# Performance work log

Hardware: AMD Instinct MI355X
Metric: run time of the kernel (lower is better)

The kernel has to match this reference:

```python
import jax, jax.numpy as jnp
import numpy as np

N_NODES = 100000
SELF_LOOP_W = 2.0  # improved=True in GCNConv -> A + 2I


def gcn_conv(x, src, dst, ew, W, b):
    """PyG GCNConv(improved=True): D^-1/2 (A + 2I) D^-1/2 X W + b.

    src/dst: edge endpoints, messages flow src -> dst (source_to_target).
    """
    n = x.shape[0]
    # degree after adding self loops with weight 2.0
    deg = jnp.zeros((n,), dtype=x.dtype).at[dst].add(ew) + SELF_LOOP_W
    dinv = jax.lax.rsqrt(deg)
    norm = dinv[src] * ew * dinv[dst]                      # [E]
    h = x @ W                                              # [N, out]
    agg = jax.ops.segment_sum(norm[:, None] * h[src], dst, num_segments=n)
    self_term = (SELF_LOOP_W * dinv * dinv)[:, None] * h   # self-loop edges
    return agg + self_term + b


def setup_inputs() -> dict:
    key = jax.random.key(0)
    ks = jax.random.split(key, 10)
    F_IN, H1, H2, C = 128, 128, 64, 5
    E = 1600000
    x = jax.random.normal(ks[0], (N_NODES, F_IN), dtype=jnp.float32)
    edge_index = jax.random.randint(ks[1], (2, E), 0, N_NODES, dtype=jnp.int64)
    edge_weight = jax.random.uniform(ks[2], (E,), dtype=jnp.float32)

    def glorot(k, shape):
        lim = float(np.sqrt(6.0 / (shape[0] + shape[1])))
        return jax.random.uniform(k, shape, jnp.float32, -lim, lim)

    return {
        "x": x,
        "edge_index": edge_index,
        "edge_weight": edge_weight,
        "W1": glorot(ks[3], (F_IN, H1)), "b1": jnp.zeros((H1,), jnp.float32),
        "W2": glorot(ks[4], (H1, H2)),  "b2": jnp.zeros((H2,), jnp.float32),
        "Wc": glorot(ks[5], (H2, C)),   "bc": jnp.zeros((C,), jnp.float32),
    }


def reference(x, edge_index, edge_weight, W1, b1, W2, b2, Wc, bc):
    src, dst = edge_index[0], edge_index[1]
    # conv1 + relu (dropout is identity in eval mode)
    h = jax.nn.relu(gcn_conv(x, src, dst, edge_weight, W1, b1))
    # conv2 + relu
    h = jax.nn.relu(gcn_conv(h, src, dst, edge_weight, W2, b2))
    # classifier head + log_softmax over classes
    logits = gcn_conv(h, src, dst, edge_weight, Wc, bc)
    return jax.nn.log_softmax(logits, axis=1)
```

## Files before the change

kernel.cpp:

```cpp
#include <hip/hip_runtime.h>
#include <hip/hip_bf16.h>

constexpr int TPB = 256;

static inline int cdiv(long long a, long long b) { return (int)((a + b - 1) / b); }

typedef __attribute__((ext_vector_type(8))) short bf16x8;
typedef __attribute__((ext_vector_type(4))) float f32x4;

__device__ inline unsigned short f2bf(float f) {
    __hip_bfloat16 h = __float2bfloat16(f);
    unsigned short u;
    __builtin_memcpy(&u, &h, 2);
    return u;
}

__device__ inline float bflo(unsigned u) { return __uint_as_float(u << 16); }
__device__ inline float bfhi(unsigned u) { return __uint_as_float(u & 0xffff0000u); }

__device__ inline unsigned relu_pk(unsigned w) {
    unsigned lo = (w & 0x8000u) ? 0u : (w & 0xFFFFu);
    unsigned hi = (w & 0x80000000u) ? 0u : (w & 0xFFFF0000u);
    return lo | hi;
}

constexpr int P1_CH   = 4096;
constexpr int MAXBINS = 512;
constexpr int BINCAP  = 4608;

__device__ __forceinline__ void part_body(const int* __restrict__ src,
                                          const int* __restrict__ dst,
                                          const float* __restrict__ ew,
                                          int* __restrict__ bincnt,
                                          int2* __restrict__ pbuf, int E, int nbins, int bid) {
    __shared__ int h[MAXBINS];
    for (int t = threadIdx.x; t < nbins; t += TPB) h[t] = 0;
    __syncthreads();
    const int lo = bid * P1_CH;
    const int hi = min(lo + P1_CH, E);
    for (int e = lo + threadIdx.x; e < hi; e += TPB)
        atomicAdd(&h[dst[e] >> 8], 1);
    __syncthreads();
    for (int t = threadIdx.x; t < nbins; t += TPB) {
        int c = h[t];
        h[t] = (c > 0) ? atomicAdd(&bincnt[t], c) : 0;
    }
    __syncthreads();
    for (int e = lo + threadIdx.x; e < hi; e += TPB) {
        int d = dst[e];
        int bin = d >> 8;
        int idx = atomicAdd(&h[bin], 1);
        if (idx < BINCAP)
            pbuf[(size_t)bin * BINCAP + idx] =
                make_int2((src[e] & 0x1FFFF) | ((d & 255) << 24), __float_as_int(ew[e]));
    }
}

template<int CAP>
__global__ __launch_bounds__(TPB) void k_bucket(const int2* __restrict__ pbuf,
                                                const int* __restrict__ bincnt,
                                                int2* __restrict__ pairs,
                                                int* __restrict__ cnt,
                                                float* __restrict__ dinv, int n) {
    __shared__ int   lcnt[TPB];
    __shared__ float ldeg[TPB];
    const int tid = threadIdx.x;
    lcnt[tid] = 0; ldeg[tid] = 0.f;
    __syncthreads();
    const int bin = blockIdx.x;
    const int m = min(bincnt[bin], BINCAP);
    const int2* pb = pbuf + (size_t)bin * BINCAP;
    for (int i = tid; i < m; i += TPB) {
        int2 pe = pb[i];
        int dlo = (pe.x >> 24) & 255;
        int s   = pe.x & 0x1FFFF;
        int pos = atomicAdd(&lcnt[dlo], 1);
        if (pos < CAP)
            pairs[(size_t)(bin * 256 + dlo) * CAP + pos] = make_int2(s, pe.y);
        atomicAdd(&ldeg[dlo], __int_as_float(pe.y));
    }
    __syncthreads();
    int node = bin * 256 + tid;
    if (node < n) {
        cnt[node]  = min(lcnt[tid], CAP);
        dinv[node] = rsqrtf(ldeg[tid] + 2.0f);
    }
}

template<int CAP>
__global__ void k_bucket_scatter(const int* __restrict__ src, const int* __restrict__ dst,
                                 const float* __restrict__ ew, int* __restrict__ cnt,
                                 int2* __restrict__ pairs, int E) {
    int e = blockIdx.x * TPB + threadIdx.x;
    if (e >= E) return;
    int d = dst[e];
    int pos = atomicAdd(&cnt[d], 1);
    if (pos < CAP)
        pairs[(size_t)d * CAP + pos] = make_int2(src[e], __float_as_int(ew[e]));
}

template<int CAP>
__global__ void k_deg(const int2* __restrict__ pairs, const int* __restrict__ cnt,
                      float* __restrict__ dinv, int n) {
    int node = blockIdx.x * (TPB / 64) + (threadIdx.x >> 6);
    if (node >= n) return;
    int lane = threadIdx.x & 63;
    int m = min(cnt[node], CAP);
    float v = 0.f;
    if (lane < m) v = __int_as_float(pairs[(size_t)node * CAP + lane].y);
#pragma unroll
    for (int d = 1; d < 64; d <<= 1) v += __shfl_xor(v, d);
    if (lane == 0) dinv[node] = rsqrtf(v + 2.0f);
}

template<int CAP>
__global__ void k_normw(int2* __restrict__ pairs, const int* __restrict__ cnt,
                        const float* __restrict__ dinv, int n) {
    int lane = threadIdx.x & 63;
    int g = lane >> 4, o = lane & 15;
    int wid = blockIdx.x * (TPB / 64) + (threadIdx.x >> 6);
    int node = wid * 4 + g;
    if (node >= n) return;
    int m = min(cnt[node], CAP);
    float dd = dinv[node];
    int2* pr = pairs + (size_t)node * CAP;
    for (int j = o; j < m; j += 16) {
        int2 p = pr[j];
        pr[j].y = __float_as_int(dinv[p.x] * __int_as_float(p.y) * dd);
    }
}


template<int KIN, int NCOL, bool RELU_IN, bool BF_IN>
__device__ __forceinline__ void gemm_mfma_body(const void* __restrict__ Xv,
                                               const float* __restrict__ W,
                                               __hip_bfloat16* __restrict__ H, int n, int bid) {
    constexpr int BM  = 128;
    constexpr int SX  = KIN + 8;
    constexpr int KCH = KIN / 32;
    constexpr int MT  = 4;
    constexpr int NT  = NCOL / 32;
    __shared__ short Xs[BM * SX];
    __shared__ short Ws[NCOL * SX];

    const int row0 = bid * BM;
    const int nrow = min(BM, n - row0);

    if constexpr (BF_IN) {
        const uint4* xg = (const uint4*)((const __hip_bfloat16*)Xv + (size_t)row0 * KIN);
        for (int i = threadIdx.x; i < BM * KIN / 8; i += TPB) {
            int r = i / (KIN / 8), c8 = i % (KIN / 8);
            uint4 v = make_uint4(0u, 0u, 0u, 0u);
            if (r < nrow) v = xg[i];
            if (RELU_IN) {
                v.x = relu_pk(v.x); v.y = relu_pk(v.y);
                v.z = relu_pk(v.z); v.w = relu_pk(v.w);
            }
            *(uint4*)&Xs[r * SX + c8 * 8] = v;
        }
    } else {
        const float4* xg = (const float4*)((const float*)Xv + (size_t)row0 * KIN);
        for (int i = threadIdx.x; i < BM * KIN / 4; i += TPB) {
            int r = i / (KIN / 4), c4 = i % (KIN / 4);
            float4 v = make_float4(0.f, 0.f, 0.f, 0.f);
            if (r < nrow) v = xg[i];
            if (RELU_IN) {
                v.x = fmaxf(v.x, 0.f); v.y = fmaxf(v.y, 0.f);
                v.z = fmaxf(v.z, 0.f); v.w = fmaxf(v.w, 0.f);
            }
            ushort4 b;
            b.x = f2bf(v.x); b.y = f2bf(v.y);
            b.z = f2bf(v.z); b.w = f2bf(v.w);
            *(ushort4*)&Xs[r * SX + c4 * 4] = b;
        }
    }
    for (int i = threadIdx.x; i < KIN * NCOL; i += TPB) {
        int k = i / NCOL, c = i % NCOL;
        Ws[c * SX + k] = (short)f2bf(W[i]);
    }
    __syncthreads();

    const int wave = threadIdx.x >> 6;
    const int lane = threadIdx.x & 63;
    const int wr = wave >> 1;
    const int wc = wave & 1;
    const int fr = lane & 15;
    const int fg = lane >> 4;

    f32x4 acc[MT][NT];
#pragma unroll
    for (int i = 0; i < MT; ++i)
#pragma unroll
        for (int j = 0; j < NT; ++j) acc[i][j] = (f32x4){0.f, 0.f, 0.f, 0.f};

    const short* xa = Xs + (wr * 64 + fr) * SX + fg * 8;
    const short* wb = Ws + (wc * NT * 16 + fr) * SX + fg * 8;

#pragma unroll
    for (int kc = 0; kc < KCH; ++kc) {
        bf16x8 a[MT], b[NT];
#pragma unroll
        for (int i = 0; i < MT; ++i)
            a[i] = *(const bf16x8*)(xa + i * 16 * SX + kc * 32);
#pragma unroll
        for (int j = 0; j < NT; ++j)
            b[j] = *(const bf16x8*)(wb + j * 16 * SX + kc * 32);
#pragma unroll
        for (int i = 0; i < MT; ++i)
#pragma unroll
            for (int j = 0; j < NT; ++j)
                acc[i][j] = __builtin_amdgcn_mfma_f32_16x16x32_bf16(a[i], b[j], acc[i][j], 0, 0, 0);
    }

#pragma unroll
    for (int i = 0; i < MT; ++i) {
#pragma unroll
        for (int j = 0; j < NT; ++j) {
            int col = wc * NT * 16 + j * 16 + fr;
            int rb  = wr * 64 + i * 16 + fg * 4;
#pragma unroll
            for (int q = 0; q < 4; ++q) {
                int r = rb + q;
                if (r < nrow)
                    H[(size_t)(row0 + r) * NCOL + col] = __float2bfloat16(acc[i][j][q]);
            }
        }
    }
}

template<int KIN, int NCOL, bool RELU_IN, bool BF_IN>
__global__ __launch_bounds__(TPB, 2) void k_gemm_mfma(const void* __restrict__ Xv,
                                                      const float* __restrict__ W,
                                                      __hip_bfloat16* __restrict__ H, int n) {
    gemm_mfma_body<KIN, NCOL, RELU_IN, BF_IN>(Xv, W, H, n, blockIdx.x);
}

__global__ __launch_bounds__(TPB, 2) void k_gemm1_part(
        const float* __restrict__ X, const float* __restrict__ W1,
        __hip_bfloat16* __restrict__ H, int n,
        const int* __restrict__ src, const int* __restrict__ dst,
        const float* __restrict__ ew, int* __restrict__ bincnt,
        int2* __restrict__ pbuf, int E, int nbins, int Gg, int Gp) {
    int b = blockIdx.x;
    int r3 = b % 3;
    if (r3 == 2) {
        int pid = b / 3;
        if (pid < Gp) part_body(src, dst, ew, bincnt, pbuf, E, nbins, pid);
    } else {
        int gid = (b / 3) * 2 + r3;
        if (gid < Gg) gemm_mfma_body<128, 128, false, false>(X, W1, H, n, gid);
    }
}

template<int KIN, int KOUT, int OSTR, bool RELU_IN>
__global__ void k_gemv(const float* __restrict__ X, const float* __restrict__ W,
                       float* __restrict__ H, int n) {
    __shared__ float ws_[KIN * KOUT];
    for (int i = threadIdx.x; i < KIN * KOUT; i += TPB) ws_[i] = W[i];
    __syncthreads();
    int r = blockIdx.x * TPB + threadIdx.x;
    if (r >= n) return;
    float acc[KOUT];
#pragma unroll
    for (int c = 0; c < KOUT; ++c) acc[c] = 0.f;
    const float4* xr = (const float4*)(X + (size_t)r * KIN);
#pragma unroll
    for (int k4 = 0; k4 < KIN / 4; ++k4) {
        float4 xv = xr[k4];
        if (RELU_IN) {
            xv.x = fmaxf(xv.x, 0.f); xv.y = fmaxf(xv.y, 0.f);
            xv.z = fmaxf(xv.z, 0.f); xv.w = fmaxf(xv.w, 0.f);
        }
        float xs[4] = {xv.x, xv.y, xv.z, xv.w};
#pragma unroll
        for (int j = 0; j < 4; ++j)
#pragma unroll
            for (int c = 0; c < KOUT; ++c)
                acc[c] = fmaf(xs[j], ws_[(k4 * 4 + j) * KOUT + c], acc[c]);
    }
#pragma unroll
    for (int c = 0; c < KOUT; ++c) H[(size_t)r * OSTR + c] = acc[c];
#pragma unroll
    for (int c = KOUT; c < OSTR; ++c) H[(size_t)r * OSTR + c] = 0.f;
}


template<int K, int CAP, bool OUT_BF16>
__global__ __launch_bounds__(TPB) void k_agg_bf(const __hip_bfloat16* __restrict__ H,
                                                const int2* __restrict__ pairs,
                                                const int* __restrict__ cnt,
                                                const float* __restrict__ dinv,
                                                const float* __restrict__ b,
                                                void* __restrict__ out, int n) {
    constexpr int LPN = K / 8;
    constexpr int GPN = 64 / LPN;
    constexpr int RQ  = K / 8;
    constexpr int NCH = CAP / 8;
    const int lane = threadIdx.x & 63;
    const int g    = lane / LPN;
    const int o    = lane % LPN;
    const int wid  = blockIdx.x * (TPB / 64) + (threadIdx.x >> 6);
    const int node = wid * GPN + g;
    const bool alive = node < n;
    const int nc = alive ? node : 0;

    const uint4* __restrict__ Hq = (const uint4*)H;

    float di   = dinv[nc];
    float coef = 2.f * di * di;
    uint4 hv = Hq[(size_t)nc * RQ + o];
    const float4* bq = (const float4*)b + o * 2;
    float4 bA = bq[0], bB = bq[1];
    float acc[8];
    acc[0] = fmaf(coef, bflo(hv.x), bA.x);
    acc[1] = fmaf(coef, bfhi(hv.x), bA.y);
    acc[2] = fmaf(coef, bflo(hv.y), bA.z);
    acc[3] = fmaf(coef, bfhi(hv.y), bA.w);
    acc[4] = fmaf(coef, bflo(hv.z), bB.x);
    acc[5] = fmaf(coef, bfhi(hv.z), bB.y);
    acc[6] = fmaf(coef, bflo(hv.w), bB.z);
    acc[7] = fmaf(coef, bfhi(hv.w), bB.w);

    const int m = alive ? min(cnt[nc], CAP) : 0;
    const int2* pp = pairs + (size_t)nc * CAP;

    uint4 Ma[4], Mb[4];
#pragma unroll
    for (int q = 0; q < 4; ++q) Ma[q] = *(const uint4*)(pp + q * 2);

    auto chunk = [&](const uint4 (&Mc)[4], uint4 (&Mn)[4], int c) {
        const int base = c * 8;
        int s[8]; float w[8];
#pragma unroll
        for (int q = 0; q < 4; ++q) {
            s[2 * q]     = (int)Mc[q].x;  w[2 * q]     = __uint_as_float(Mc[q].y);
            s[2 * q + 1] = (int)Mc[q].z;  w[2 * q + 1] = __uint_as_float(Mc[q].w);
        }
        uint4 r[8];
#pragma unroll
        for (int u = 0; u < 8; ++u) {
            bool ok = (base + u) < m;
            int ss = ok ? s[u] : 0;
            if (!ok) w[u] = 0.f;
            r[u] = Hq[(size_t)ss * RQ + o];
        }
        if (base + 8 < m) {
#pragma unroll
            for (int q = 0; q < 4; ++q) Mn[q] = *(const uint4*)(pp + base + 8 + q * 2);
        }
#pragma unroll
        for (int u = 0; u < 8; ++u) {
            acc[0] = fmaf(w[u], bflo(r[u].x), acc[0]);
            acc[1] = fmaf(w[u], bfhi(r[u].x), acc[1]);
            acc[2] = fmaf(w[u], bflo(r[u].y), acc[2]);
            acc[3] = fmaf(w[u], bfhi(r[u].y), acc[3]);
            acc[4] = fmaf(w[u], bflo(r[u].z), acc[4]);
            acc[5] = fmaf(w[u], bfhi(r[u].z), acc[5]);
            acc[6] = fmaf(w[u], bflo(r[u].w), acc[6]);
            acc[7] = fmaf(w[u], bfhi(r[u].w), acc[7]);
        }
    };

#pragma unroll
    for (int c = 0; c < NCH; c += 2) {
        if (c * 8 >= m) break;
        chunk(Ma, Mb, c);
        if ((c + 1) * 8 >= m) break;
        chunk(Mb, Ma, c + 1);
    }

    if (alive) {
        if constexpr (OUT_BF16) {
            unsigned p0 = (unsigned)f2bf(acc[0]) | ((unsigned)f2bf(acc[1]) << 16);
            unsigned p1 = (unsigned)f2bf(acc[2]) | ((unsigned)f2bf(acc[3]) << 16);
            unsigned p2 = (unsigned)f2bf(acc[4]) | ((unsigned)f2bf(acc[5]) << 16);
            unsigned p3 = (unsigned)f2bf(acc[6]) | ((unsigned)f2bf(acc[7]) << 16);
            ((uint4*)out)[(size_t)node * RQ + o] = make_uint4(p0, p1, p2, p3);
        } else {
            float4* ap = (float4*)out + (size_t)node * (K / 4) + o * 2;
            ap[0] = make_float4(acc[0], acc[1], acc[2], acc[3]);
            ap[1] = make_float4(acc[4], acc[5], acc[6], acc[7]);
        }
    }
}

template<int CAP>
__global__ void k_agg5_lsm(const float* __restrict__ H, const int2* __restrict__ pairs,
                           const int* __restrict__ cnt, const float* __restrict__ dinv,
                           const float* __restrict__ b, float* __restrict__ out, int n) {
    constexpr int NCH = CAP / 8;
    int i = blockIdx.x * TPB + threadIdx.x;
    const bool alive = i < n;
    const int nc = alive ? i : 0;
    float di = dinv[nc];
    float coef = 2.f * di * di;
    float acc[5];
    {
        const float4 h0 = *(const float4*)(H + (size_t)nc * 8);
        const float  h4 = H[(size_t)nc * 8 + 4];
        acc[0] = fmaf(coef, h0.x, b[0]);
        acc[1] = fmaf(coef, h0.y, b[1]);
        acc[2] = fmaf(coef, h0.z, b[2]);
        acc[3] = fmaf(coef, h0.w, b[3]);
        acc[4] = fmaf(coef, h4,   b[4]);
    }
    const int m = alive ? min(cnt[nc], CAP) : 0;
    const int2* pp = pairs + (size_t)nc * CAP;

    uint4 Ma[4], Mb[4];
#pragma unroll
    for (int q = 0; q < 4; ++q) Ma[q] = *(const uint4*)(pp + q * 2);

    auto chunk = [&](const uint4 (&Mc)[4], uint4 (&Mn)[4], int c) {
        const int base = c * 8;
        int s[8]; float w[8];
#pragma unroll
        for (int q = 0; q < 4; ++q) {
            s[2 * q]     = (int)Mc[q].x;  w[2 * q]     = __uint_as_float(Mc[q].y);
            s[2 * q + 1] = (int)Mc[q].z;  w[2 * q + 1] = __uint_as_float(Mc[q].w);
        }
        float4 q0[8]; float q4[8];
#pragma unroll
        for (int u = 0; u < 8; ++u) {
            bool ok = (base + u) < m;
            int ss = ok ? s[u] : 0;
            if (!ok) w[u] = 0.f;
            const float* h = H + (size_t)ss * 8;
            q0[u] = *(const float4*)h;
            q4[u] = h[4];
        }
        if (base + 8 < m) {
#pragma unroll
            for (int q = 0; q < 4; ++q) Mn[q] = *(const uint4*)(pp + base + 8 + q * 2);
        }
#pragma unroll
        for (int u = 0; u < 8; ++u) {
            acc[0] = fmaf(w[u], q0[u].x, acc[0]);
            acc[1] = fmaf(w[u], q0[u].y, acc[1]);
            acc[2] = fmaf(w[u], q0[u].z, acc[2]);
            acc[3] = fmaf(w[u], q0[u].w, acc[3]);
            acc[4] = fmaf(w[u], q4[u],   acc[4]);
        }
    };

#pragma unroll
    for (int c = 0; c < NCH; c += 2) {
        if (c * 8 >= m) break;
        chunk(Ma, Mb, c);
        if ((c + 1) * 8 >= m) break;
        chunk(Mb, Ma, c + 1);
    }

    if (alive) {
        float mx = acc[0];
#pragma unroll
        for (int c = 1; c < 5; ++c) mx = fmaxf(mx, acc[c]);
        float ssum = 0.f;
#pragma unroll
        for (int c = 0; c < 5; ++c) ssum += expf(acc[c] - mx);
        float lg = mx + logf(ssum);
#pragma unroll
        for (int c = 0; c < 5; ++c) out[(size_t)i * 5 + c] = acc[c] - lg;
    }
}


template<int CAP>
static void run_all(const float* x, const int* srcv, const int* dstv, const float* ew,
                    const float* W1, const float* b1, const float* W2, const float* b2,
                    const float* Wc, const float* bc, float* out,
                    int n, int E, char* p, hipStream_t stream) {
    auto alloc = [&](size_t bytes) {
        char* r = p;
        p += (bytes + 255) & ~(size_t)255;
        return r;
    };
    float*          dinv   = (float*)alloc((size_t)n * 4);
    int*            cnt    = (int*)alloc((size_t)n * 4);
    int2*           pairs  = (int2*)alloc((size_t)n * CAP * 8);
    __hip_bfloat16* Hbf    = (__hip_bfloat16*)alloc((size_t)n * 128 * 2);
    __hip_bfloat16* A1bf   = (__hip_bfloat16*)alloc((size_t)n * 128 * 2);
    float*          bufB   = (float*)alloc((size_t)n * 64 * 4);
    float*          H3     = (float*)alloc((size_t)n * 8 * 4);
    int*            bincnt = (int*)alloc((size_t)MAXBINS * 4);
    int2*           pbuf   = (int2*)alloc((size_t)MAXBINS * BINCAP * 8);

    const int WPB = TPB / 64;
    const int nbins = cdiv(n, 256);

    if (nbins <= MAXBINS) {
        (void)hipMemsetAsync(bincnt, 0, (size_t)nbins * 4, stream);
        int Gg = cdiv(n, 128);
        int Gp = cdiv(E, P1_CH);
        int Gh = cdiv(Gg, 2);
        int G  = 3 * (Gp > Gh ? Gp : Gh);
        k_gemm1_part<<<G, TPB, 0, stream>>>(x, W1, Hbf, n, srcv, dstv, ew,
                                            bincnt, pbuf, E, nbins, Gg, Gp);
        k_bucket<CAP><<<nbins, TPB, 0, stream>>>(pbuf, bincnt, pairs, cnt, dinv, n);
    } else {
        (void)hipMemsetAsync(cnt, 0, (size_t)n * 4, stream);
        k_bucket_scatter<CAP><<<cdiv(E, TPB), TPB, 0, stream>>>(srcv, dstv, ew, cnt, pairs, E);
        k_deg<CAP><<<cdiv(n, WPB), TPB, 0, stream>>>(pairs, cnt, dinv, n);
        k_gemm_mfma<128, 128, false, false><<<cdiv(n, 128), TPB, 0, stream>>>(x, W1, Hbf, n);
    }
    k_normw<CAP><<<cdiv(n, WPB * 4), TPB, 0, stream>>>(pairs, cnt, dinv, n);

    k_agg_bf<128, CAP, true><<<cdiv(n, WPB * 4), TPB, 0, stream>>>(Hbf, pairs, cnt, dinv, b1, A1bf, n);

    k_gemm_mfma<128, 64, true, true><<<cdiv(n, 128), TPB, 0, stream>>>(A1bf, W2, Hbf, n);
    k_agg_bf<64, CAP, false><<<cdiv(n, WPB * 8), TPB, 0, stream>>>(Hbf, pairs, cnt, dinv, b2, bufB, n);

    k_gemv<64, 5, 8, true><<<cdiv(n, TPB), TPB, 0, stream>>>(bufB, Wc, H3, n);
    k_agg5_lsm<CAP><<<cdiv(n, TPB), TPB, 0, stream>>>(H3, pairs, cnt, dinv, bc, out, n);
}

extern "C" void kernel_launch(void* const* d_in, const int* in_sizes, int n_in,
                              void* d_out, int out_size, void* d_ws, size_t ws_size,
                              hipStream_t stream) {
    const float* x  = (const float*)d_in[0];
    const int*   ei = (const int*)d_in[1];
    const float* ew = (const float*)d_in[2];
    const float* W1 = (const float*)d_in[3];
    const float* b1 = (const float*)d_in[4];
    const float* W2 = (const float*)d_in[5];
    const float* b2 = (const float*)d_in[6];
    const float* Wc = (const float*)d_in[7];
    const float* bc = (const float*)d_in[8];

    const int E   = in_sizes[2];
    const int H1  = in_sizes[4];
    const int FIN = in_sizes[3] / H1;
    const int n   = in_sizes[0] / FIN;

    const int* srcv = ei;
    const int* dstv = ei + E;

    size_t fixed = ((size_t)n * 4 + 256) * 2 + ((size_t)n * 128 * 2 + 256) * 2 +
                   (size_t)n * 64 * 4 + 256 + (size_t)n * 8 * 4 + 256 +
                   (size_t)MAXBINS * 4 + 256 + (size_t)MAXBINS * BINCAP * 8 + 256 + 1024;
    if (ws_size == 0 || ws_size >= fixed + (size_t)n * 64 * 8)
        run_all<64>(x, srcv, dstv, ew, W1, b1, W2, b2, Wc, bc, (float*)d_out, n, E,
                    (char*)d_ws, stream);
    else
        run_all<48>(x, srcv, dstv, ew, W1, b1, W2, b2, Wc, bc, (float*)d_out, n, E,
                    (char*)d_ws, stream);
}
```

Measured before the change: 217.0 us.

## Drop normalized-weight pass, compute edge norms in aggregation, stage bucket writes in LDS

Removes the k_normw pass that rewrote each edge weight as dinv[src]*w*dinv[dst]. The three aggregation kernels now gather dinv[src] per edge and apply the normalization inline. k_bucket now does a prefix scan and stages edges in shared memory so the writes to pairs are contiguous rather than atomic-scattered. The fused gemm1+partition kernel is split back into separate launches, which gives up the overlap it provided but frees the bucket kernel's larger shared-memory use. The trade is an extra random dinv gather per edge in each of three layers, against one fewer full pass over the edge list.

After: 231.3 us. 1.07x slower.

```diff
diff --git a/kernel.cpp b/kernel.cpp
--- a/kernel.cpp
+++ b/kernel.cpp
@@ -28,15 +28,15 @@
 constexpr int MAXBINS = 512;
 constexpr int BINCAP  = 4608;
 
-__device__ __forceinline__ void part_body(const int* __restrict__ src,
-                                          const int* __restrict__ dst,
-                                          const float* __restrict__ ew,
-                                          int* __restrict__ bincnt,
-                                          int2* __restrict__ pbuf, int E, int nbins, int bid) {
+__global__ __launch_bounds__(TPB) void k_part(const int* __restrict__ src,
+                                              const int* __restrict__ dst,
+                                              const float* __restrict__ ew,
+                                              int* __restrict__ bincnt,
+                                              int2* __restrict__ pbuf, int E, int nbins) {
     __shared__ int h[MAXBINS];
     for (int t = threadIdx.x; t < nbins; t += TPB) h[t] = 0;
     __syncthreads();
-    const int lo = bid * P1_CH;
+    const int lo = blockIdx.x * P1_CH;
     const int hi = min(lo + P1_CH, E);
     for (int e = lo + threadIdx.x; e < hi; e += TPB)
         atomicAdd(&h[dst[e] >> 8], 1);
@@ -62,10 +62,15 @@
                                                 int2* __restrict__ pairs,
                                                 int* __restrict__ cnt,
                                                 float* __restrict__ dinv, int n) {
-    __shared__ int   lcnt[TPB];
-    __shared__ float ldeg[TPB];
+    __shared__ int   lcnt[256];
+    __shared__ int   loff[256];
+    __shared__ int   posc[256];
+    __shared__ float ldeg[256];
+    __shared__ int   scan_[256];
+    __shared__ int2  sbuf[BINCAP];
+    __shared__ unsigned char dbin[BINCAP];
     const int tid = threadIdx.x;
-    lcnt[tid] = 0; ldeg[tid] = 0.f;
+    lcnt[tid] = 0; ldeg[tid] = 0.f; posc[tid] = 0;
     __syncthreads();
     const int bin = blockIdx.x;
     const int m = min(bincnt[bin], BINCAP);
@@ -73,16 +78,42 @@
     for (int i = tid; i < m; i += TPB) {
         int2 pe = pb[i];
         int dlo = (pe.x >> 24) & 255;
-        int s   = pe.x & 0x1FFFF;
-        int pos = atomicAdd(&lcnt[dlo], 1);
-        if (pos < CAP)
-            pairs[(size_t)(bin * 256 + dlo) * CAP + pos] = make_int2(s, pe.y);
+        atomicAdd(&lcnt[dlo], 1);
         atomicAdd(&ldeg[dlo], __int_as_float(pe.y));
     }
     __syncthreads();
+    const int c = min(lcnt[tid], CAP);
+    scan_[tid] = c;
+    __syncthreads();
+#pragma unroll
+    for (int off = 1; off < 256; off <<= 1) {
+        int t = 0;
+        if (tid >= off) t = scan_[tid - off];
+        __syncthreads();
+        if (tid >= off) scan_[tid] += t;
+        __syncthreads();
+    }
+    loff[tid] = scan_[tid] - c;
+    __syncthreads();
+    const int total = scan_[255];
+    for (int i = tid; i < m; i += TPB) {
+        int2 pe = pb[i];
+        int dlo = (pe.x >> 24) & 255;
+        int slot = atomicAdd(&posc[dlo], 1);
+        if (slot < CAP) {
+            int j = loff[dlo] + slot;
+            sbuf[j] = make_int2(pe.x & 0x1FFFF, pe.y);
+            dbin[j] = (unsigned char)dlo;
+        }
+    }
+    __syncthreads();
+    for (int j = tid; j < total; j += TPB) {
+        int dlo = dbin[j];
+        pairs[(size_t)(bin * 256 + dlo) * CAP + (j - loff[dlo])] = sbuf[j];
+    }
     int node = bin * 256 + tid;
     if (node < n) {
-        cnt[node]  = min(lcnt[tid], CAP);
+        cnt[node]  = c;
         dinv[node] = rsqrtf(ldeg[tid] + 2.0f);
     }
 }
@@ -113,28 +144,11 @@
     if (lane == 0) dinv[node] = rsqrtf(v + 2.0f);
 }
 
-template<int CAP>
-__global__ void k_normw(int2* __restrict__ pairs, const int* __restrict__ cnt,
-                        const float* __restrict__ dinv, int n) {
-    int lane = threadIdx.x & 63;
-    int g = lane >> 4, o = lane & 15;
-    int wid = blockIdx.x * (TPB / 64) + (threadIdx.x >> 6);
-    int node = wid * 4 + g;
-    if (node >= n) return;
-    int m = min(cnt[node], CAP);
-    float dd = dinv[node];
-    int2* pr = pairs + (size_t)node * CAP;
-    for (int j = o; j < m; j += 16) {
-        int2 p = pr[j];
-        pr[j].y = __float_as_int(dinv[p.x] * __int_as_float(p.y) * dd);
-    }
-}
-
 
 template<int KIN, int NCOL, bool RELU_IN, bool BF_IN>
-__device__ __forceinline__ void gemm_mfma_body(const void* __restrict__ Xv,
-                                               const float* __restrict__ W,
-                                               __hip_bfloat16* __restrict__ H, int n, int bid) {
+__global__ __launch_bounds__(TPB, 2) void k_gemm_mfma(const void* __restrict__ Xv,
+                                                      const float* __restrict__ W,
+                                                      __hip_bfloat16* __restrict__ H, int n) {
     constexpr int BM  = 128;
     constexpr int SX  = KIN + 8;
     constexpr int KCH = KIN / 32;
@@ -143,7 +157,7 @@
     __shared__ short Xs[BM * SX];
     __shared__ short Ws[NCOL * SX];
 
-    const int row0 = bid * BM;
+    const int row0 = blockIdx.x * BM;
     const int nrow = min(BM, n - row0);
 
     if constexpr (BF_IN) {
@@ -225,30 +239,6 @@
                     H[(size_t)(row0 + r) * NCOL + col] = __float2bfloat16(acc[i][j][q]);
             }
         }
-    }
-}
-
-template<int KIN, int NCOL, bool RELU_IN, bool BF_IN>
-__global__ __launch_bounds__(TPB, 2) void k_gemm_mfma(const void* __restrict__ Xv,
-                                                      const float* __restrict__ W,
-                                                      __hip_bfloat16* __restrict__ H, int n) {
-    gemm_mfma_body<KIN, NCOL, RELU_IN, BF_IN>(Xv, W, H, n, blockIdx.x);
-}
-
-__global__ __launch_bounds__(TPB, 2) void k_gemm1_part(
-        const float* __restrict__ X, const float* __restrict__ W1,
-        __hip_bfloat16* __restrict__ H, int n,
-        const int* __restrict__ src, const int* __restrict__ dst,
-        const float* __restrict__ ew, int* __restrict__ bincnt,
-        int2* __restrict__ pbuf, int E, int nbins, int Gg, int Gp) {
-    int b = blockIdx.x;
-    int r3 = b % 3;
-    if (r3 == 2) {
-        int pid = b / 3;
-        if (pid < Gp) part_body(src, dst, ew, bincnt, pbuf, E, nbins, pid);
-    } else {
-        int gid = (b / 3) * 2 + r3;
-        if (gid < Gg) gemm_mfma_body<128, 128, false, false>(X, W1, H, n, gid);
     }
 }
 
@@ -330,19 +320,21 @@
 
     auto chunk = [&](const uint4 (&Mc)[4], uint4 (&Mn)[4], int c) {
         const int base = c * 8;
-        int s[8]; float w[8];
+        int s[8]; float we[8];
 #pragma unroll
         for (int q = 0; q < 4; ++q) {
-            s[2 * q]     = (int)Mc[q].x;  w[2 * q]     = __uint_as_float(Mc[q].y);
-            s[2 * q + 1] = (int)Mc[q].z;  w[2 * q + 1] = __uint_as_float(Mc[q].w);
-        }
+            s[2 * q]     = (int)Mc[q].x;  we[2 * q]     = __uint_as_float(Mc[q].y);
+            s[2 * q + 1] = (int)Mc[q].z;  we[2 * q + 1] = __uint_as_float(Mc[q].w);
+        }
+        float dv[8];
         uint4 r[8];
 #pragma unroll
         for (int u = 0; u < 8; ++u) {
             bool ok = (base + u) < m;
             int ss = ok ? s[u] : 0;
-            if (!ok) w[u] = 0.f;
-            r[u] = Hq[(size_t)ss * RQ + o];
+            if (!ok) we[u] = 0.f;
+            dv[u] = dinv[ss];
+            r[u]  = Hq[(size_t)ss * RQ + o];
         }
         if (base + 8 < m) {
 #pragma unroll
@@ -350,14 +342,15 @@
         }
 #pragma unroll
         for (int u = 0; u < 8; ++u) {
-            acc[0] = fmaf(w[u], bflo(r[u].x), acc[0]);
-            acc[1] = fmaf(w[u], bfhi(r[u].x), acc[1]);
-            acc[2] = fmaf(w[u], bflo(r[u].y), acc[2]);
-            acc[3] = fmaf(w[u], bfhi(r[u].y), acc[3]);
-            acc[4] = fmaf(w[u], bflo(r[u].z), acc[4]);
-            acc[5] = fmaf(w[u], bfhi(r[u].z), acc[5]);
-            acc[6] = fmaf(w[u], bflo(r[u].w), acc[6]);
-            acc[7] = fmaf(w[u], bfhi(r[u].w), acc[7]);
+            float w = dv[u] * we[u] * di;
+            acc[0] = fmaf(w, bflo(r[u].x), acc[0]);
+            acc[1] = fmaf(w, bfhi(r[u].x), acc[1]);
+            acc[2] = fmaf(w, bflo(r[u].y), acc[2]);
+            acc[3] = fmaf(w, bfhi(r[u].y), acc[3]);
+            acc[4] = fmaf(w, bflo(r[u].z), acc[4]);
+            acc[5] = fmaf(w, bfhi(r[u].z), acc[5]);
+            acc[6] = fmaf(w, bflo(r[u].w), acc[6]);
+            acc[7] = fmaf(w, bfhi(r[u].w), acc[7]);
         }
     };
 
@@ -413,18 +406,20 @@
 
     auto chunk = [&](const uint4 (&Mc)[4], uint4 (&Mn)[4], int c) {
         const int base = c * 8;
-        int s[8]; float w[8];
+        int s[8]; float we[8];
 #pragma unroll
         for (int q = 0; q < 4; ++q) {
-            s[2 * q]     = (int)Mc[q].x;  w[2 * q]     = __uint_as_float(Mc[q].y);
-            s[2 * q + 1] = (int)Mc[q].z;  w[2 * q + 1] = __uint_as_float(Mc[q].w);
-        }
+            s[2 * q]     = (int)Mc[q].x;  we[2 * q]     = __uint_as_float(Mc[q].y);
+            s[2 * q + 1] = (int)Mc[q].z;  we[2 * q + 1] = __uint_as_float(Mc[q].w);
+        }
+        float dv[8];
         float4 q0[8]; float q4[8];
 #pragma unroll
         for (int u = 0; u < 8; ++u) {
             bool ok = (base + u) < m;
             int ss = ok ? s[u] : 0;
-            if (!ok) w[u] = 0.f;
+            if (!ok) we[u] = 0.f;
+            dv[u] = dinv[ss];
             const float* h = H + (size_t)ss * 8;
             q0[u] = *(const float4*)h;
             q4[u] = h[4];
@@ -435,11 +430,12 @@
         }
 #pragma unroll
         for (int u = 0; u < 8; ++u) {
-            acc[0] = fmaf(w[u], q0[u].x, acc[0]);
-            acc[1] = fmaf(w[u], q0[u].y, acc[1]);
-            acc[2] = fmaf(w[u], q0[u].z, acc[2]);
-            acc[3] = fmaf(w[u], q0[u].w, acc[3]);
-            acc[4] = fmaf(w[u], q4[u],   acc[4]);
+            float w = dv[u] * we[u] * di;
+            acc[0] = fmaf(w, q0[u].x, acc[0]);
+            acc[1] = fmaf(w, q0[u].y, acc[1]);
+            acc[2] = fmaf(w, q0[u].z, acc[2]);
+            acc[3] = fmaf(w, q0[u].w, acc[3]);
+            acc[4] = fmaf(w, q4[u],   acc[4]);
         }
     };
 
@@ -490,21 +486,15 @@
 
     if (nbins <= MAXBINS) {
         (void)hipMemsetAsync(bincnt, 0, (size_t)nbins * 4, stream);
-        int Gg = cdiv(n, 128);
-        int Gp = cdiv(E, P1_CH);
-        int Gh = cdiv(Gg, 2);
-        int G  = 3 * (Gp > Gh ? Gp : Gh);
-        k_gemm1_part<<<G, TPB, 0, stream>>>(x, W1, Hbf, n, srcv, dstv, ew,
-                                            bincnt, pbuf, E, nbins, Gg, Gp);
+        k_part<<<cdiv(E, P1_CH), TPB, 0, stream>>>(srcv, dstv, ew, bincnt, pbuf, E, nbins);
         k_bucket<CAP><<<nbins, TPB, 0, stream>>>(pbuf, bincnt, pairs, cnt, dinv, n);
     } else {
         (void)hipMemsetAsync(cnt, 0, (size_t)n * 4, stream);
         k_bucket_scatter<CAP><<<cdiv(E, TPB), TPB, 0, stream>>>(srcv, dstv, ew, cnt, pairs, E);
         k_deg<CAP><<<cdiv(n, WPB), TPB, 0, stream>>>(pairs, cnt, dinv, n);
-        k_gemm_mfma<128, 128, false, false><<<cdiv(n, 128), TPB, 0, stream>>>(x, W1, Hbf, n);
-    }
-    k_normw<CAP><<<cdiv(n, WPB * 4), TPB, 0, stream>>>(pairs, cnt, dinv, n);
-
+    }
+
+    k_gemm_mfma<128, 128, false, false><<<cdiv(n, 128), TPB, 0, stream>>>(x, W1, Hbf, n);
     k_agg_bf<128, CAP, true><<<cdiv(n, WPB * 4), TPB, 0, stream>>>(Hbf, pairs, cnt, dinv, b1, A1bf, n);
 
     k_gemm_mfma<128, 64, true, true><<<cdiv(n, 128), TPB, 0, stream>>>(A1bf, W2, Hbf, n);
```
